# Performance work log

Hardware: AMD Instinct MI355X
Metric: run time of the kernel (lower is better)

Reference implementation:

```python
import jax, jax.numpy as jnp
import numpy as np

IMAGE_SIZE = 640
NUM_CLASSES = 80
MAX_BOXES = 100
SCORE_THR = 0.25
IOU_THR = 0.1
K_PRE = 256  # pre-NMS candidates per class (fixed-shape surrogate for tf.where filtering)
ANCHORS = np.array([[10,13],[16,30],[33,23],[30,61],[62,45],[59,119],
                    [116,90],[156,198],[373,326]], dtype=np.float32)


def setup_inputs() -> dict:
    key = jax.random.key(0)
    k5, k4, k3 = jax.random.split(key, 3)
    B = 16
    return {
        "p5": jax.random.normal(k5, (B, 20, 20, 255), dtype=jnp.float32),
        "p4": jax.random.normal(k4, (B, 40, 40, 255), dtype=jnp.float32),
        "p3": jax.random.normal(k3, (B, 80, 80, 255), dtype=jnp.float32),
    }


def _decode_layer(fm, anchors):
    # fm: [B, g, g, 3*(5+C)]; anchors: [3, 2] in input-image pixels
    B, g = fm.shape[0], fm.shape[1]
    ratio = IMAGE_SIZE / g
    fm = fm.reshape(B, g, g, 3, 5 + NUM_CLASSES)
    ctr = jax.nn.sigmoid(fm[..., :2])                      # [B,g,g,3,2]
    gx, gy = jnp.meshgrid(jnp.arange(g), jnp.arange(g))    # 'xy' indexing, same as tf
    offset = jnp.stack([gx, gy], axis=-1).astype(fm.dtype)[:, :, None, :]
    ctr = (ctr + offset) * ratio                           # pixel-space centers (x, y)
    # (anchor/ratio)*exp(t)*ratio == anchor*exp(t)
    sizes = jnp.exp(fm[..., 2:4]) * anchors                # pixel-space (w, h)
    conf = jax.nn.sigmoid(fm[..., 4:5])
    prob = jax.nn.sigmoid(fm[..., 5:])
    boxes = jnp.concatenate([ctr, sizes], axis=-1).reshape(B, -1, 4)
    scores = (conf * prob).reshape(B, -1, NUM_CLASSES)
    return boxes, scores


def _pairwise_iou(b):
    # b: [K, 4] in (x1, y1, x2, y2)
    x1, y1, x2, y2 = b[:, 0], b[:, 1], b[:, 2], b[:, 3]
    area = jnp.maximum(x2 - x1, 0.0) * jnp.maximum(y2 - y1, 0.0)
    iw = jnp.maximum(jnp.minimum(x2[:, None], x2[None, :]) - jnp.maximum(x1[:, None], x1[None, :]), 0.0)
    ih = jnp.maximum(jnp.minimum(y2[:, None], y2[None, :]) - jnp.maximum(y1[:, None], y1[None, :]), 0.0)
    inter = iw * ih
    union = area[:, None] + area[None, :] - inter
    return inter / jnp.maximum(union, 1e-9)


def _nms_class(boxes, scores):
    # boxes: [N,4], scores: [N] for one class of one image
    s = jnp.where(scores > SCORE_THR, scores, -1.0)
    top_s, top_i = jax.lax.top_k(s, K_PRE)        # score-sorted candidates
    cb = jnp.take(boxes, top_i, axis=0)           # [K_PRE, 4]
    iou = _pairwise_iou(cb)                       # [K_PRE, K_PRE]
    idx = jnp.arange(K_PRE)
    supp0 = top_s <= SCORE_THR                    # below-threshold slots start suppressed

    def body(i, supp):
        alive = ~supp[i]
        return supp | (alive & (iou[i] > IOU_THR) & (idx > i))

    supp = jax.lax.fori_loop(0, K_PRE, body, supp0)
    keep = ~supp
    # tf NMS caps output at MAX_BOXES per class (boxes are score-sorted)
    keep = keep & (jnp.cumsum(keep.astype(jnp.int32)) <= MAX_BOXES)
    kept_s = jnp.where(keep, top_s, -1.0)
    return kept_s, top_i


def _nms_image(boxes, scores):
    # boxes: [N,4], scores: [N,C]
    kept_s, top_i = jax.vmap(_nms_class, in_axes=(None, 1))(boxes, scores)  # [C,K],[C,K]
    flat_s = kept_s.reshape(-1)
    flat_i = top_i.reshape(-1)
    cls = jnp.repeat(jnp.arange(NUM_CLASSES), K_PRE)
    fs, fi = jax.lax.top_k(flat_s, MAX_BOXES)     # global top-k across all classes
    box_idx = flat_i[fi]
    valid = fs > 0.0                              # padded/suppressed slots carry -1
    out_boxes = jnp.where(valid[:, None], jnp.take(boxes, box_idx, axis=0), -1.0)
    out_scores = jnp.where(valid, fs, -1.0)
    out_labels = jnp.where(valid, cls[fi], -1).astype(jnp.int32)
    return out_boxes, out_scores, out_labels


def reference(p5, p4, p3):
    b5, s5 = _decode_layer(p5, ANCHORS[6:9])
    b4, s4 = _decode_layer(p4, ANCHORS[3:6])
    b3, s3 = _decode_layer(p3, ANCHORS[0:3])
    boxes = jnp.concatenate([b5, b4, b3], axis=1)   # [B, 25200, 4] (cx, cy, w, h)
    scores = jnp.concatenate([s5, s4, s3], axis=1)  # [B, 25200, 80]
    cx, cy, w, h = boxes[..., 0], boxes[..., 1], boxes[..., 2], boxes[..., 3]
    boxes = jnp.stack([cx - w / 2, cy - h / 2, cx + w / 2, cy + h / 2], axis=-1)
    return jax.vmap(_nms_image)(boxes, scores)      # ([B,100,4], [B,100], [B,100] int32)
```

## Files before the change

kernel.cpp:

```cpp
#include <hip/hip_runtime.h>
#include <cstdint>

#define NBOX 25200
#define NCLS 80
#define NIMG 16
#define KPRE 256
#define MAXB 100
#define SCORE_THR 0.25f
#define IOU_THR 0.1f
#define GCAP 512
#define GCAP_OLD 2048
#define NBINS_OLD 4096
#define FK 512
#define LCAP 3072
#define SCAP 24
#define CSTR 16
#define CUT 0.5f
#define BINW 0.001953125f
#define HS2 512.0f
#define RSC 262144.0f
#define BPI 394
#define FBBINS 2048

__constant__ float c_AW[9] = {10.f,16.f,33.f,30.f,62.f,59.f,116.f,156.f,373.f};
__constant__ float c_AH[9] = {13.f,30.f,23.f,61.f,45.f,119.f,90.f,198.f,326.f};

__device__ __forceinline__ float sigmoidf_(float x) { return 1.0f / (1.0f + expf(-x)); }

__device__ __forceinline__ void box_loc(int i, const float* p5, const float* p4, const float* p3,
                                        const float*& p, int& g, int& li, int& abase) {
  if (i < 1200)      { p = p5; g = 20; li = i;        abase = 6; }
  else if (i < 6000) { p = p4; g = 40; li = i - 1200; abase = 3; }
  else               { p = p3; g = 80; li = i - 6000; abase = 0; }
}

__device__ __forceinline__ float score_full(const float* p5, const float* p4, const float* p3,
                                            int b, int c, int i) {
  const float* p; int g, li, abase;
  box_loc(i, p5, p4, p3, p, g, li, abase);
  const float* f = p + (size_t)((size_t)b * g * g * 3 + li) * 85;
  return __fmul_rn(sigmoidf_(f[4]), sigmoidf_(f[5 + c]));
}

__global__ __launch_bounds__(512) void decode_push_kernel(
    const float* __restrict__ p5, const float* __restrict__ p4, const float* __restrict__ p3,
    float* __restrict__ boxes, unsigned long long* __restrict__ lists,
    uint32_t* __restrict__ cnts, uint32_t* __restrict__ ovfl)
{
  __shared__ float rec[64 * 85];
  __shared__ float conf_s[64];
  __shared__ unsigned long long slist[NCLS][SCAP];
  __shared__ uint32_t wcnt[NCLS];
  __shared__ uint32_t sbase[NCLS], sst[NCLS];
  __shared__ unsigned short pairbuf[8 * 64];

  const int bi = blockIdx.x;
  const int b = bi / BPI, r = bi - b * BPI;
  const float* p; int g, lb, s0, nb, abase;
  if (r < 19)      { p = p5; g = 20; lb = 0;    s0 = r * 64;        abase = 6; nb = 1200  - s0; }
  else if (r < 94) { p = p4; g = 40; lb = 1200; s0 = (r - 19) * 64; abase = 3; nb = 4800  - s0; }
  else             { p = p3; g = 80; lb = 6000; s0 = (r - 94) * 64; abase = 0; nb = 19200 - s0; }
  if (nb > 64) nb = 64;
  const int tid = threadIdx.x;

  if (tid < NCLS) wcnt[tid] = 0;
  {
    const float4* src4 = (const float4*)(p + ((size_t)b * g * g * 3 + s0) * 85);
    float4* rec4 = (float4*)rec;
    int n4 = nb * 85 / 4;
    for (int k = tid; k < n4; k += 512) rec4[k] = src4[k];
  }
  __syncthreads();

  if (tid < nb) {
    const float* f = rec + tid * 85;
    int li = s0 + tid;
    int cell = li / 3, a = li - cell * 3;
    float ratio = 640.0f / (float)g;
    float cx = (sigmoidf_(f[0]) + (float)(cell % g)) * ratio;
    float cy = (sigmoidf_(f[1]) + (float)(cell / g)) * ratio;
    float w = expf(f[2]) * c_AW[abase + a];
    float h = expf(f[3]) * c_AH[abase + a];
    float hw = 0.5f * w, hh = 0.5f * h;
    float4* ob = (float4*)(boxes + ((size_t)b * NBOX + lb + li) * 4);
    *ob = make_float4(cx - hw, cy - hh, cx + hw, cy + hh);
    conf_s[tid] = sigmoidf_(f[4]);
  }
  __syncthreads();

  {
    const int wave = tid >> 6, lane = tid & 63;
    const int c0 = wave * 10;
    const bool jok = lane < nb;
    float cl = jok ? rec[lane * 85 + 4] : -1.0f;
    float Lthr;
    if (!jok || cl <= 0.0f) {
      Lthr = 3.0e38f;
    } else {
      float conf = conf_s[lane];
      float u = CUT / conf;
      if (u > 0.999f) Lthr = -3.0e38f;
      else Lthr = logf(u / (1.0f - u)) - 0.01f;
    }
    const float* fl = rec + lane * 85 + 5;
    const unsigned long long lt = (lane == 0) ? 0ull : (~0ull >> (64 - lane));
    unsigned short* pb = pairbuf + (wave << 6);

    auto flushFn = [&](int mm) {
      if (lane < mm) {
        int e = pb[lane];
        int l2 = e >> 4, cc2 = e & 15;
        int c2 = c0 + cc2;
        float s = __fmul_rn(conf_s[l2], sigmoidf_(rec[l2 * 85 + 5 + c2]));
        if (s > CUT) {
          uint32_t slot = atomicAdd(&wcnt[c2], 1u);
          if (slot < SCAP)
            slist[c2][slot] = ((unsigned long long)__float_as_uint(s) << 32)
                              | (0xFFFFFFFFu - (uint32_t)(lb + s0 + l2));
        }
      }
    };

    int m = 0;
    for (int cc = 0; cc < 10; ++cc) {
      float lg = jok ? fl[c0 + cc] : -3.0e38f;
      bool cand = lg > Lthr;
      unsigned long long mk = __ballot(cand);
      int pc = __popcll(mk);
      if (m + pc > 64) { flushFn(m); m = 0; }
      if (cand) {
        int rank = __popcll(mk & lt);
        pb[m + rank] = (unsigned short)((lane << 4) | cc);
      }
      m += pc;
    }
    flushFn(m);
  }
  __syncthreads();

  if (tid < NCLS) {
    uint32_t full = wcnt[tid];
    if (full > SCAP) ovfl[b * NCLS + tid] = 1u;
    uint32_t st = full < SCAP ? full : SCAP;
    sst[tid] = st;
    sbase[tid] = atomicAdd(&cnts[(size_t)(b * NCLS + tid) * CSTR], st);
  }
  __syncthreads();

  for (int t = tid; t < NCLS * SCAP; t += 512) {
    int c = t / SCAP, k = t - c * SCAP;
    if ((uint32_t)k < sst[c]) {
      uint32_t dst = sbase[c] + (uint32_t)k;
      if (dst < LCAP)
        lists[(size_t)(b * NCLS + c) * LCAP + dst] = slist[c][k];
    }
  }
}

union ShMix2 {
  uint32_t rhist[512];
  uint32_t fhist[FBBINS];
  unsigned long long rowm[KPRE][4];
};

__global__ __launch_bounds__(512) void select_nms_list_kernel(
    const unsigned long long* __restrict__ lists, const uint32_t* __restrict__ cnts,
    const uint32_t* __restrict__ ovfl, const float* __restrict__ boxes,
    const float* __restrict__ p5, const float* __restrict__ p4, const float* __restrict__ p3,
    float* __restrict__ kept_s, int* __restrict__ top_i)
{
  const int task = blockIdx.x;
  const int b = task / NCLS, c = task - b * NCLS;
  const int tid = threadIdx.x;

  __shared__ uint32_t S[256];
  __shared__ unsigned long long keys[GCAP];
  __shared__ ShMix2 u;
  __shared__ float4 bbx[KPRE];
  __shared__ float bar_[KPRE];
  __shared__ unsigned long long suppInit[4];
  __shared__ unsigned long long sh_t[4];
  __shared__ int s_B, s_cnt, s_state, sh_stop;
  __shared__ float s_gl, s_lo, s_hi;
  __shared__ uint32_t s_above, s_g2;

  const uint32_t cntraw = cnts[(size_t)task * CSTR];
  bool fb = (ovfl[task] != 0u) || !(cntraw >= (uint32_t)KPRE && cntraw <= (uint32_t)LCAP);
  float thr = CUT;
  int n_all = (int)(cntraw < (uint32_t)LCAP ? cntraw : (uint32_t)LCAP);
  const unsigned long long* gl = lists + (size_t)task * LCAP;

  if (!fb && n_all > 500) {
    if (tid < 256) S[tid] = 0;
    __syncthreads();
    for (int z = tid; z < n_all; z += 512) {
      float s = __uint_as_float((uint32_t)(gl[z] >> 32));
      int bin = (int)(__fmul_rn(__fsub_rn(s, CUT), HS2));
      bin = bin < 0 ? 0 : (bin > 255 ? 255 : bin);
      atomicAdd(&S[bin], 1u);
    }
    __syncthreads();
    for (int off = 1; off < 256; off <<= 1) {
      uint32_t add = 0;
      if (tid < 256 && tid + off < 256) add = S[tid + off];
      __syncthreads();
      if (tid < 256) S[tid] += add;
      __syncthreads();
    }
    if (tid == 0) s_B = 0;
    __syncthreads();
    if (tid < 256) {
      uint32_t Sz = S[tid];
      uint32_t Sz1 = (tid < 255) ? S[tid + 1] : 0u;
      if (Sz >= KPRE && (tid == 255 || Sz1 < KPRE)) s_B = tid;
    }
    __syncthreads();
    const int B = s_B;
    const uint32_t gcount = S[B];
    const uint32_t aboveB = (B < 255) ? S[B + 1] : 0u;
    thr = CUT + (float)B * BINW;
    if (gcount > 500u) {
      for (int z = tid; z < 512; z += 512) u.rhist[z] = 0u;
      __syncthreads();
      float rLo = thr;
      for (int z = tid; z < n_all; z += 512) {
        float s = __uint_as_float((uint32_t)(gl[z] >> 32));
        int bin = (int)(__fmul_rn(__fsub_rn(s, CUT), HS2));
        bin = bin < 0 ? 0 : (bin > 255 ? 255 : bin);
        if (bin == B) {
          int sub = (int)((s - rLo) * RSC);
          sub = sub < 0 ? 0 : (sub > 511 ? 511 : sub);
          atomicAdd(&u.rhist[sub], 1u);
        }
      }
      __syncthreads();
// ... 73 lines not shown
  __syncthreads();
  if (!fb) {
    for (int z = tid; z < n_all; z += 512) {
      unsigned long long kk = gl[z];
      float s = __uint_as_float((uint32_t)(kk >> 32));
      if (s > thr_n) {
        int slot = atomicAdd(&s_cnt, 1);
        if (slot < GCAP) keys[slot] = kk;
      }
    }
  } else {
    for (int i = tid; i < NBOX; i += 512) {
      float s = score_full(p5, p4, p3, b, c, i);
      if (s > thr_n && s > SCORE_THR) {
        int slot = atomicAdd(&s_cnt, 1);
        if (slot < GCAP)
          keys[slot] = ((unsigned long long)__float_as_uint(s) << 32) | (0xFFFFFFFFu - (uint32_t)i);
      }
    }
  }
  __syncthreads();
  int n = s_cnt < GCAP ? s_cnt : GCAP;
  if (tid >= n) keys[tid] = 0ull;
  __syncthreads();
  {
    unsigned long long v = keys[tid];
    for (int k = 2; k <= GCAP; k <<= 1) {
      for (int j = k >> 1; j > 0; j >>= 1) {
        unsigned long long pv;
        if (j >= 64) {
          keys[tid] = v;
          __syncthreads();
          pv = keys[tid ^ j];
          __syncthreads();
        } else {
          pv = __shfl_xor(v, j, 64);
        }
        bool takeMax = (((tid & k) == 0) == ((tid & j) == 0));
        v = takeMax ? (v > pv ? v : pv) : (v < pv ? v : pv);
      }
    }
    keys[tid] = v;
  }
  __syncthreads();

  const int col = tid & 255;
  float sc; int idx;
  {
    unsigned long long kk = keys[col];
    if ((uint32_t)(kk >> 32) != 0u) { sc = __uint_as_float((uint32_t)(kk >> 32)); idx = (int)(0xFFFFFFFFu - (uint32_t)kk); }
    else { sc = -1.0f; idx = 0; }
  }
  if (tid < KPRE) {
    const float* bp = boxes + ((size_t)b * NBOX + idx) * 4;
    float bx1 = bp[0], by1 = bp[1], bx2 = bp[2], by2 = bp[3];
    bbx[tid] = make_float4(bx1, by1, bx2, by2);
    bar_[tid] = __fmul_rn(fmaxf(__fsub_rn(bx2, bx1), 0.0f), fmaxf(__fsub_rn(by2, by1), 0.0f));
  }
  {
    unsigned long long alive = __ballot(sc > SCORE_THR);
    if (tid < KPRE && (tid & 63) == 0) suppInit[tid >> 6] = ~alive;
  }
  if (tid == 0) sh_stop = 0;
  __syncthreads();
  float4 MB = bbx[col];
  float x1 = MB.x, y1 = MB.y, x2 = MB.z, y2 = MB.w;
  float area = bar_[col];
  if (tid < 4) sh_t[tid] = suppInit[tid];
  __syncthreads();

  int P = 4;
  const int rg = tid >> 8;
  #pragma unroll
  for (int q = 0; q < 4; ++q) {
    for (int ii = 0; ii < 64; ii += 2) {
      int i = q * 64 + ii + rg;
      if (!((sh_t[q] >> (ii + rg)) & 1ull)) {
        float4 B = bbx[i];
        float ar = bar_[i];
        float iw = fmaxf(__fsub_rn(fminf(x2, B.z), fmaxf(x1, B.x)), 0.0f);
        float ih = fmaxf(__fsub_rn(fminf(y2, B.w), fmaxf(y1, B.y)), 0.0f);
        float inter = __fmul_rn(iw, ih);
        float ab = __fadd_rn(ar, area);
        float diff = __fsub_rn(__fmul_rn(inter, 1.1f), __fmul_rn(0.1f, ab));
        bool sup;
        if (fabsf(diff) > 1e-5f * ab) {
          sup = diff > 0.0f;
        } else {
          float uni = __fsub_rn(ab, inter);
          sup = (inter / fmaxf(uni, 1e-9f)) > IOU_THR;
        }
        sup = sup && (col > i);
        unsigned long long m = __ballot(sup);
        if ((tid & 63) == 0) u.rowm[i][(tid >> 6) & 3] = m;
      }
    }
    __syncthreads();
    if (tid == 0) {
      unsigned long long t0 = sh_t[0], t1 = sh_t[1], t2 = sh_t[2], t3 = sh_t[3];
      for (int ii = 0; ii < 64; ++ii) {
        int i = q * 64 + ii;
        unsigned long long cur = (q == 0) ? t0 : (q == 1) ? t1 : (q == 2) ? t2 : t3;
        if (!((cur >> ii) & 1ull)) {
          if (q <= 0) t0 |= u.rowm[i][0];
          if (q <= 1) t1 |= u.rowm[i][1];
          if (q <= 2) t2 |= u.rowm[i][2];
          t3 |= u.rowm[i][3];
        }
      }
      sh_t[0] = t0; sh_t[1] = t1; sh_t[2] = t2; sh_t[3] = t3;
      int kept = __popcll(~t0);
      if (q >= 1) kept += __popcll(~t1);
      if (q >= 2) kept += __popcll(~t2);
      if (q >= 3) kept += __popcll(~t3);
      if (kept >= MAXB) sh_stop = 1;
    }
    __syncthreads();
    if (sh_stop) { P = q + 1; break; }
  }

  if (tid < KPRE) {
    unsigned long long tw = sh_t[tid >> 6];
    bool kept = (tid < 64 * P) && !((tw >> (tid & 63)) & 1ull);
    int rank = 0;
    #pragma unroll
    for (int w2 = 0; w2 < 4; ++w2)
      if (w2 < (tid >> 6)) rank += __popcll(~sh_t[w2]);
    int l = tid & 63;
    rank += (l == 0) ? 0 : __popcll(~tw & ((~0ull) >> (64 - l)));
    bool fin = kept && (rank < MAXB);
    kept_s[(size_t)task * KPRE + tid] = fin ? sc : -1.0f;
    top_i[(size_t)task * KPRE + tid] = idx;
  }
}

__global__ __launch_bounds__(256) void decode_kernel(
    const float* __restrict__ p5, const float* __restrict__ p4, const float* __restrict__ p3,
    float* __restrict__ boxes, float* __restrict__ conf)
{
  int t = blockIdx.x * 256 + threadIdx.x;
  if (t >= NIMG * NBOX) return;
  int b = t / NBOX, i = t - b * NBOX;
  const float* p; int g, li, abase;
  box_loc(i, p5, p4, p3, p, g, li, abase);
  int cell = li / 3, a = li - cell * 3;
  float ratio = 640.0f / (float)g;
  const float* f = p + ((size_t)((size_t)b * g * g + cell) * 255 + a * 85);
  float cx = (sigmoidf_(f[0]) + (float)(cell % g)) * ratio;
  float cy = (sigmoidf_(f[1]) + (float)(cell / g)) * ratio;
  float w = expf(f[2]) * c_AW[abase + a];
  float h = expf(f[3]) * c_AH[abase + a];
  float hw = 0.5f * w, hh = 0.5f * h;
  float* ob = boxes + (size_t)t * 4;
  ob[0] = cx - hw; ob[1] = cy - hh; ob[2] = cx + hw; ob[3] = cy + hh;
  conf[t] = sigmoidf_(f[4]);
}

__device__ __forceinline__ float score_at(
    const float* __restrict__ p5, const float* __restrict__ p4, const float* __restrict__ p3,
    const float* __restrict__ conf, int b, int c, int i)
{
  const float* p; int g, li, abase;
  box_loc(i, p5, p4, p3, p, g, li, abase);
  float logit = p[(size_t)((size_t)b * g * g * 3 + li) * 85 + 5 + c];
  return __fmul_rn(conf[b * NBOX + i], 1.0f / (1.0f + expf(-logit)));
}

__global__ __launch_bounds__(256) void select_nms_kernel(
    const float* __restrict__ p5, const float* __restrict__ p4, const float* __restrict__ p3,
    const float* __restrict__ conf, const float* __restrict__ boxes,
    float* __restrict__ kept_s, int* __restrict__ top_i)
{
  const int task = blockIdx.x;
  const int b = task / NCLS, c = task - b * NCLS;
  const int tid = threadIdx.x;
  __shared__ uint32_t hist[NBINS_OLD];
  __shared__ uint32_t chunkS[256];
  __shared__ unsigned long long keys[GCAP_OLD];
  __shared__ float s_lo, s_hi, s_glo;
  __shared__ uint32_t s_above;
  __shared__ int s_state, s_cnt;

  float lo = SCORE_THR, hi = 1.0f;
  uint32_t above = 0;
  float gatherLo = SCORE_THR;
  bool done = false;
  for (int iter = 0; iter < 6 && !done; ++iter) {
    for (int z = tid; z < NBINS_OLD; z += 256) hist[z] = 0;
    __syncthreads();
    float scale = (float)NBINS_OLD / (hi - lo);
    for (int i = tid; i < NBOX; i += 256) {
      float s = score_at(p5, p4, p3, conf, b, c, i);
      if (s > lo && s <= hi) {
        int bin = (int)((s - lo) * scale);
        bin = bin < 0 ? 0 : (bin > NBINS_OLD - 1 ? NBINS_OLD - 1 : bin);
        atomicAdd(&hist[bin], 1u);
      }
    }
    __syncthreads();
    { uint32_t cs = 0; int base = tid * 16;
      #pragma unroll
      for (int z = 0; z < 16; ++z) cs += hist[base + z];
      chunkS[tid] = cs; }
    __syncthreads();
    if (tid == 0) {
      uint32_t acc = 0; int ch;
      for (ch = 255; ch >= 0; --ch) {
        if (above + acc + chunkS[ch] >= KPRE) break;
// ... 42 lines not shown
          unsigned long long a0 = keys[i2], b0_ = keys[ixj];
          bool sw = ((i2 & k) == 0) ? (a0 < b0_) : (a0 > b0_);
          if (sw) { keys[i2] = b0_; keys[ixj] = a0; }
        }
      }
      __syncthreads();
    }
  }
  __shared__ float bx1[KPRE], by1[KPRE], bx2[KPRE], by2[KPRE], bar_[KPRE], tsc[KPRE];
  __shared__ int tix[KPRE];
  __shared__ unsigned char suppA[KPRE], keepA[KPRE];
  { int r = tid;
    unsigned long long kk = keys[r];
    float sc; int idx;
    if ((uint32_t)(kk >> 32) != 0u) { sc = __uint_as_float((uint32_t)(kk >> 32)); idx = (int)(0xFFFFFFFFu - (uint32_t)kk); }
    else { sc = -1.0f; idx = 0; }
    tsc[r] = sc; tix[r] = idx;
    const float* bp = boxes + ((size_t)b * NBOX + idx) * 4;
    float x1 = bp[0], y1 = bp[1], x2 = bp[2], y2 = bp[3];
    bx1[r] = x1; by1[r] = y1; bx2[r] = x2; by2[r] = y2;
    bar_[r] = __fmul_rn(fmaxf(__fsub_rn(x2, x1), 0.0f), fmaxf(__fsub_rn(y2, y1), 0.0f));
    suppA[r] = (sc <= SCORE_THR) ? 1 : 0; }
  __syncthreads();
  for (int i = 0; i < KPRE; ++i) {
    if (suppA[i] == 0) {
      int r = tid;
      if (r > i) {
        float iw = fmaxf(__fsub_rn(fminf(bx2[r], bx2[i]), fmaxf(bx1[r], bx1[i])), 0.0f);
        float ih = fmaxf(__fsub_rn(fminf(by2[r], by2[i]), fmaxf(by1[r], by1[i])), 0.0f);
        float inter = __fmul_rn(iw, ih);
        float uni = __fsub_rn(__fadd_rn(bar_[r], bar_[i]), inter);
        float iou = inter / fmaxf(uni, 1e-9f);
        if (iou > IOU_THR) suppA[r] = 1;
      }
    }
    __syncthreads();
  }
  if (tid == 0) {
    int cnt = 0;
    for (int r = 0; r < KPRE; ++r) {
      int kp = (suppA[r] == 0) ? 1 : 0;
      if (kp && cnt < MAXB) cnt++; else kp = 0;
      keepA[r] = (unsigned char)kp;
    }
  }
  __syncthreads();
  { int r = tid;
    kept_s[(size_t)task * KPRE + r] = keepA[r] ? tsc[r] : -1.0f;
    top_i[(size_t)task * KPRE + r] = tix[r]; }
}

__global__ __launch_bounds__(256) void final_topk_kernel(
    const float* __restrict__ kept_s, const int* __restrict__ top_i,
    const float* __restrict__ boxes, float* __restrict__ out)
{
  int b = blockIdx.x, tid = threadIdx.x;
  __shared__ uint32_t hist[NBINS_OLD];
  __shared__ uint32_t chunkS[256];
  __shared__ unsigned long long keys[FK];
  __shared__ float s_lo, s_hi, s_glo;
  __shared__ uint32_t s_above;
  __shared__ int s_state, s_cnt;
  const float* ks = kept_s + (size_t)b * NCLS * KPRE;
  const int NK = NCLS * KPRE;

  float lo = SCORE_THR, hi = 1.0f;
  uint32_t above = 0;
  float gatherLo = SCORE_THR;
  bool done = false;

  for (int iter = 0; iter < 4 && !done; ++iter) {
    for (int z = tid; z < NBINS_OLD; z += 256) hist[z] = 0;
    __syncthreads();
    float scale = (float)NBINS_OLD / (hi - lo);
    for (int z = tid; z < NK; z += 256) {
      float s = ks[z];
      if (s > lo && s <= hi) {
        int bin = (int)((s - lo) * scale);
        bin = bin < 0 ? 0 : (bin > NBINS_OLD - 1 ? NBINS_OLD - 1 : bin);
        atomicAdd(&hist[bin], 1u);
      }
    }
    __syncthreads();
    {
      uint32_t cs = 0; int base = tid * 16;
      #pragma unroll
      for (int z = 0; z < 16; ++z) cs += hist[base + z];
      chunkS[tid] = cs;
    }
    __syncthreads();
    if (tid == 0) {
      uint32_t acc = 0; int ch;
      for (ch = 255; ch >= 0; --ch) {
        if (above + acc + chunkS[ch] >= MAXB) break;
        acc += chunkS[ch];
      }
      if (ch < 0) { s_state = 1; s_glo = SCORE_THR; }
      else {
        int B = -1;
        for (int z = ch * 16 + 15; z >= ch * 16; --z) {
          acc += hist[z];
          if (above + acc >= MAXB) { B = z; break; }
        }
        uint32_t popB = hist[B];
        uint32_t aboveNew = above + acc - popB;
        float wdt = (hi - lo) / (float)NBINS_OLD;
        float binLo = lo + (float)B * wdt;
        if (aboveNew + popB <= (uint32_t)(FK - 64) || iter == 3) { s_state = 1; s_glo = binLo; }
        else { s_state = 0; s_lo = binLo; s_hi = binLo + wdt; s_above = aboveNew; }
      }
    }
    __syncthreads();
    if (s_state == 1) { gatherLo = s_glo; done = true; }
    else { lo = s_lo; hi = s_hi; above = s_above; }
    __syncthreads();
  }
  gatherLo = __uint_as_float(__float_as_uint(gatherLo) - 8u);

  if (tid == 0) s_cnt = 0;
  __syncthreads();
  for (int z = tid; z < NK; z += 256) {
    float s = ks[z];
    if (s > gatherLo && s > 0.0f) {
      int slot = atomicAdd(&s_cnt, 1);
      if (slot < FK)
        keys[slot] = ((unsigned long long)__float_as_uint(s) << 32) | (uint32_t)(0xFFFFFFFFu - (uint32_t)z);
    }
  }
  __syncthreads();
  int n = s_cnt < FK ? s_cnt : FK;
  for (int z = tid; z < FK; z += 256) if (z >= n) keys[z] = 0ull;
  __syncthreads();
  for (int k = 2; k <= FK; k <<= 1) {
    for (int j = k >> 1; j > 0; j >>= 1) {
      for (int i2 = tid; i2 < FK; i2 += 256) {
        int ixj = i2 ^ j;
        if (ixj > i2) {
          unsigned long long a0 = keys[i2], b0_ = keys[ixj];
          bool sw = ((i2 & k) == 0) ? (a0 < b0_) : (a0 > b0_);
          if (sw) { keys[i2] = b0_; keys[ixj] = a0; }
        }
      }
      __syncthreads();
    }
  }
  float* ob = out + (size_t)b * MAXB * 4;
  float* os = out + (size_t)NIMG * MAXB * 4 + (size_t)b * MAXB;
  float* ol = out + (size_t)NIMG * MAXB * 4 + (size_t)NIMG * MAXB + (size_t)b * MAXB;
  for (int t = tid; t < MAXB; t += 256) {
    unsigned long long kk = keys[t];
    if ((uint32_t)(kk >> 32) != 0u) {
      float s = __uint_as_float((uint32_t)(kk >> 32));
      int fr = (int)(0xFFFFFFFFu - (uint32_t)kk);
      int cc = fr >> 8, rr = fr & 255;
      int idx = top_i[((size_t)b * NCLS + cc) * KPRE + rr];
      const float* bp = boxes + ((size_t)b * NBOX + idx) * 4;
      ob[t * 4 + 0] = bp[0]; ob[t * 4 + 1] = bp[1]; ob[t * 4 + 2] = bp[2]; ob[t * 4 + 3] = bp[3];
      os[t] = s; ol[t] = (float)cc;
    } else {
      ob[t * 4 + 0] = -1.0f; ob[t * 4 + 1] = -1.0f; ob[t * 4 + 2] = -1.0f; ob[t * 4 + 3] = -1.0f;
      os[t] = -1.0f; ol[t] = -1.0f;
    }
  }
}

extern "C" void kernel_launch(void* const* d_in, const int* in_sizes, int n_in,
                              void* d_out, int out_size, void* d_ws, size_t ws_size,
                              hipStream_t stream)
{
  const float* p5 = (const float*)d_in[0];
  const float* p4 = (const float*)d_in[1];
  const float* p3 = (const float*)d_in[2];
  float* out = (float*)d_out;

  float*    boxes = (float*)d_ws;
  float*    kept  = boxes + (size_t)NIMG * NBOX * 4;
  int*      topi  = (int*)(kept + (size_t)NIMG * NCLS * KPRE);
  uint32_t* cnts  = (uint32_t*)(topi + (size_t)NIMG * NCLS * KPRE);
  uint32_t* ovfl  = cnts + (size_t)NIMG * NCLS * CSTR;
  unsigned long long* lists = (unsigned long long*)(ovfl + NIMG * NCLS);

  size_t need_main = ((size_t)NIMG * NBOX * 4 + (size_t)NIMG * NCLS * KPRE * 2
                      + (size_t)NIMG * NCLS * CSTR + (size_t)NIMG * NCLS) * 4
                     + (size_t)NIMG * NCLS * LCAP * 8;

  if (ws_size >= need_main) {
    hipMemsetAsync(cnts, 0, (size_t)NIMG * NCLS * (CSTR + 1) * sizeof(uint32_t), stream);
    decode_push_kernel<<<NIMG * BPI, 512, 0, stream>>>(p5, p4, p3, boxes, lists, cnts, ovfl);
    select_nms_list_kernel<<<NIMG * NCLS, 512, 0, stream>>>(lists, cnts, ovfl, boxes, p5, p4, p3, kept, topi);
  } else {
    float* conf = (float*)(cnts);
    decode_kernel<<<(NIMG * NBOX + 255) / 256, 256, 0, stream>>>(p5, p4, p3, boxes, conf);
    select_nms_kernel<<<NIMG * NCLS, 256, 0, stream>>>(p5, p4, p3, conf, boxes, kept, topi);
  }
  final_topk_kernel<<<NIMG, 256, 0, stream>>>(kept, topi, boxes, out);
}
```

Measured before the change: 209.9 us.

## Decode boxes on demand and fuse final top-k into last NMS block

Stops materialising the full decoded box array in the decode kernel. Boxes are recomputed from the raw feature maps only for the candidates NMS and the output need. The final per-image top-k is folded into the select/NMS kernel through a last-block-done atomic counter, which removes one kernel launch. The serial single-thread suppression scan becomes a wave-wide scan using shuffles. In exchange it adds redundant sigmoid/exp work, a threadfence and atomic per block, and a serial tail done by the last block of each image.

```diff
diff --git a/kernel.cpp b/kernel.cpp
--- a/kernel.cpp
+++ b/kernel.cpp
@@ -42,13 +42,27 @@
   return __fmul_rn(sigmoidf_(f[4]), sigmoidf_(f[5 + c]));
 }
 
+__device__ __forceinline__ float4 decode_box(const float* p5, const float* p4, const float* p3,
+                                             int b, int i) {
+  const float* p; int g, li, abase;
+  box_loc(i, p5, p4, p3, p, g, li, abase);
+  const float* f = p + (size_t)((size_t)b * g * g * 3 + li) * 85;
+  int cell = li / 3, a = li - cell * 3;
+  float ratio = 640.0f / (float)g;
+  float cx = (sigmoidf_(f[0]) + (float)(cell % g)) * ratio;
+  float cy = (sigmoidf_(f[1]) + (float)(cell / g)) * ratio;
+  float w = expf(f[2]) * c_AW[abase + a];
+  float h = expf(f[3]) * c_AH[abase + a];
+  float hw = 0.5f * w, hh = 0.5f * h;
+  return make_float4(cx - hw, cy - hh, cx + hw, cy + hh);
+}
+
 __global__ __launch_bounds__(512) void decode_push_kernel(
     const float* __restrict__ p5, const float* __restrict__ p4, const float* __restrict__ p3,
-    float* __restrict__ boxes, unsigned long long* __restrict__ lists,
-    uint32_t* __restrict__ cnts, uint32_t* __restrict__ ovfl)
+    unsigned long long* __restrict__ lists, uint32_t* __restrict__ cnts,
+    uint32_t* __restrict__ ovfl)
 {
   __shared__ float rec[64 * 85];
-  __shared__ float conf_s[64];
   __shared__ unsigned long long slist[NCLS][SCAP];
   __shared__ uint32_t wcnt[NCLS];
   __shared__ uint32_t sbase[NCLS], sst[NCLS];
@@ -56,10 +70,10 @@
 
   const int bi = blockIdx.x;
   const int b = bi / BPI, r = bi - b * BPI;
-  const float* p; int g, lb, s0, nb, abase;
-  if (r < 19)      { p = p5; g = 20; lb = 0;    s0 = r * 64;        abase = 6; nb = 1200  - s0; }
-  else if (r < 94) { p = p4; g = 40; lb = 1200; s0 = (r - 19) * 64; abase = 3; nb = 4800  - s0; }
-  else             { p = p3; g = 80; lb = 6000; s0 = (r - 94) * 64; abase = 0; nb = 19200 - s0; }
+  const float* p; int g, lb, s0, nb;
+  if (r < 19)      { p = p5; g = 20; lb = 0;    s0 = r * 64;        nb = 1200  - s0; }
+  else if (r < 94) { p = p4; g = 40; lb = 1200; s0 = (r - 19) * 64; nb = 4800  - s0; }
+  else             { p = p3; g = 80; lb = 6000; s0 = (r - 94) * 64; nb = 19200 - s0; }
   if (nb > 64) nb = 64;
   const int tid = threadIdx.x;
 
@@ -69,22 +83,6 @@
     float4* rec4 = (float4*)rec;
     int n4 = nb * 85 / 4;
     for (int k = tid; k < n4; k += 512) rec4[k] = src4[k];
-  }
-  __syncthreads();
-
-  if (tid < nb) {
-    const float* f = rec + tid * 85;
-    int li = s0 + tid;
-    int cell = li / 3, a = li - cell * 3;
-    float ratio = 640.0f / (float)g;
-    float cx = (sigmoidf_(f[0]) + (float)(cell % g)) * ratio;
-    float cy = (sigmoidf_(f[1]) + (float)(cell / g)) * ratio;
-    float w = expf(f[2]) * c_AW[abase + a];
-    float h = expf(f[3]) * c_AH[abase + a];
-    float hw = 0.5f * w, hh = 0.5f * h;
-    float4* ob = (float4*)(boxes + ((size_t)b * NBOX + lb + li) * 4);
-    *ob = make_float4(cx - hw, cy - hh, cx + hw, cy + hh);
-    conf_s[tid] = sigmoidf_(f[4]);
   }
   __syncthreads();
 
@@ -97,10 +95,10 @@
     if (!jok || cl <= 0.0f) {
       Lthr = 3.0e38f;
     } else {
-      float conf = conf_s[lane];
-      float u = CUT / conf;
-      if (u > 0.999f) Lthr = -3.0e38f;
-      else Lthr = logf(u / (1.0f - u)) - 0.01f;
+      float conf = 1.0f / (1.0f + expf(-cl));
+      float u2 = CUT / conf;
+      if (u2 > 0.999f) Lthr = -3.0e38f;
+      else Lthr = logf(u2 / (1.0f - u2)) - 0.01f;
     }
     const float* fl = rec + lane * 85 + 5;
     const unsigned long long lt = (lane == 0) ? 0ull : (~0ull >> (64 - lane));
@@ -111,7 +109,7 @@
         int e = pb[lane];
         int l2 = e >> 4, cc2 = e & 15;
         int c2 = c0 + cc2;
-        float s = __fmul_rn(conf_s[l2], sigmoidf_(rec[l2 * 85 + 5 + c2]));
+        float s = __fmul_rn(sigmoidf_(rec[l2 * 85 + 4]), sigmoidf_(rec[l2 * 85 + 5 + c2]));
         if (s > CUT) {
           uint32_t slot = atomicAdd(&wcnt[c2], 1u);
           if (slot < SCAP)
@@ -165,9 +163,10 @@
 
 __global__ __launch_bounds__(512) void select_nms_list_kernel(
     const unsigned long long* __restrict__ lists, const uint32_t* __restrict__ cnts,
-    const uint32_t* __restrict__ ovfl, const float* __restrict__ boxes,
+    const uint32_t* __restrict__ ovfl,
     const float* __restrict__ p5, const float* __restrict__ p4, const float* __restrict__ p3,
-    float* __restrict__ kept_s, int* __restrict__ top_i)
+    float* __restrict__ kept_s, int* __restrict__ top_i,
+    uint32_t* __restrict__ imgcnt, float* __restrict__ out)
 {
   const int task = blockIdx.x;
   const int b = task / NCLS, c = task - b * NCLS;
@@ -180,7 +179,7 @@
   __shared__ float bar_[KPRE];
   __shared__ unsigned long long suppInit[4];
   __shared__ unsigned long long sh_t[4];
-  __shared__ int s_B, s_cnt, s_state, sh_stop;
+  __shared__ int s_B, s_cnt, s_state, sh_stop, sh_last;
   __shared__ float s_gl, s_lo, s_hi;
   __shared__ uint32_t s_above, s_g2;
 
@@ -360,10 +359,9 @@
     else { sc = -1.0f; idx = 0; }
   }
   if (tid < KPRE) {
-    const float* bp = boxes + ((size_t)b * NBOX + idx) * 4;
-    float bx1 = bp[0], by1 = bp[1], bx2 = bp[2], by2 = bp[3];
-    bbx[tid] = make_float4(bx1, by1, bx2, by2);
-    bar_[tid] = __fmul_rn(fmaxf(__fsub_rn(bx2, bx1), 0.0f), fmaxf(__fsub_rn(by2, by1), 0.0f));
+    float4 bx = decode_box(p5, p4, p3, b, idx);
+    bbx[tid] = bx;
+    bar_[tid] = __fmul_rn(fmaxf(__fsub_rn(bx.z, bx.x), 0.0f), fmaxf(__fsub_rn(bx.w, bx.y), 0.0f));
   }
   {
     unsigned long long alive = __ballot(sc > SCORE_THR);
@@ -404,24 +402,28 @@
       }
     }
     __syncthreads();
-    if (tid == 0) {
+    if (tid < 64) {
+      unsigned long long r0 = u.rowm[q * 64 + tid][0];
+      unsigned long long r1 = u.rowm[q * 64 + tid][1];
+      unsigned long long r2 = u.rowm[q * 64 + tid][2];
+      unsigned long long r3 = u.rowm[q * 64 + tid][3];
       unsigned long long t0 = sh_t[0], t1 = sh_t[1], t2 = sh_t[2], t3 = sh_t[3];
+      unsigned long long tq = (q == 0) ? t0 : (q == 1) ? t1 : (q == 2) ? t2 : t3;
       for (int ii = 0; ii < 64; ++ii) {
-        int i = q * 64 + ii;
-        unsigned long long cur = (q == 0) ? t0 : (q == 1) ? t1 : (q == 2) ? t2 : t3;
-        if (!((cur >> ii) & 1ull)) {
-          if (q <= 0) t0 |= u.rowm[i][0];
-          if (q <= 1) t1 |= u.rowm[i][1];
-          if (q <= 2) t2 |= u.rowm[i][2];
-          t3 |= u.rowm[i][3];
-        }
-      }
-      sh_t[0] = t0; sh_t[1] = t1; sh_t[2] = t2; sh_t[3] = t3;
-      int kept = __popcll(~t0);
-      if (q >= 1) kept += __popcll(~t1);
-      if (q >= 2) kept += __popcll(~t2);
-      if (q >= 3) kept += __popcll(~t3);
-      if (kept >= MAXB) sh_stop = 1;
+        if (!((tq >> ii) & 1ull)) {
+          t0 |= __shfl(r0, ii); t1 |= __shfl(r1, ii);
+          t2 |= __shfl(r2, ii); t3 |= __shfl(r3, ii);
+          tq = (q == 0) ? t0 : (q == 1) ? t1 : (q == 2) ? t2 : t3;
+        }
+      }
+      if (tid == 0) {
+        sh_t[0] = t0; sh_t[1] = t1; sh_t[2] = t2; sh_t[3] = t3;
+        int kept = __popcll(~t0);
+        if (q >= 1) kept += __popcll(~t1);
+        if (q >= 2) kept += __popcll(~t2);
+        if (q >= 3) kept += __popcll(~t3);
+        if (kept >= MAXB) sh_stop = 1;
+      }
     }
     __syncthreads();
     if (sh_stop) { P = q + 1; break; }
@@ -440,6 +442,125 @@
     kept_s[(size_t)task * KPRE + tid] = fin ? sc : -1.0f;
     top_i[(size_t)task * KPRE + tid] = idx;
   }
+
+  __threadfence();
+  __syncthreads();
+  if (tid == 0) {
+    uint32_t done = atomicAdd(&imgcnt[b], 1u);
+    sh_last = (done == (uint32_t)(NCLS - 1)) ? 1 : 0;
+  }
+  __syncthreads();
+  if (!sh_last) return;
+  __threadfence();
+
+  const float* ks = kept_s + (size_t)b * NCLS * KPRE;
+  const int NK = NCLS * KPRE;
+  {
+    float lo = SCORE_THR, hi = 1.0f;
+    uint32_t above = 0;
+    float gLo = SCORE_THR;
+    bool done2 = false;
+    for (int iter = 0; iter < 4 && !done2; ++iter) {
+      for (int z = tid; z < FBBINS; z += 512) u.fhist[z] = 0u;
+      __syncthreads();
+      float scale = (float)FBBINS / (hi - lo);
+      for (int z = tid; z < NK; z += 512) {
+        float s = ks[z];
+        if (s > lo && s <= hi) {
+          int bin = (int)((s - lo) * scale);
+          bin = bin < 0 ? 0 : (bin > FBBINS - 1 ? FBBINS - 1 : bin);
+          atomicAdd(&u.fhist[bin], 1u);
+        }
+      }
+      __syncthreads();
+      if (tid < 256) {
+        uint32_t cs = 0; int base = tid * 8;
+        #pragma unroll
+        for (int z = 0; z < 8; ++z) cs += u.fhist[base + z];
+        S[tid] = cs;
+      }
+      __syncthreads();
+      if (tid == 0) {
+        uint32_t acc = 0; int ch;
+        for (ch = 255; ch >= 0; --ch) {
+          if (above + acc + S[ch] >= MAXB) break;
+          acc += S[ch];
+        }
+        if (ch < 0) { s_state = 1; s_gl = SCORE_THR; }
+        else {
+          int B = -1;
+          for (int z = ch * 8 + 7; z >= ch * 8; --z) {
+            acc += u.fhist[z];
+            if (above + acc >= MAXB) { B = z; break; }
+          }
+          uint32_t popB = u.fhist[B];
+          uint32_t aboveNew = above + acc - popB;
+          float wdt = (hi - lo) / (float)FBBINS;
+          float binLo = lo + (float)B * wdt;
+          if (aboveNew + popB <= (uint32_t)(FK - 64) || iter == 3) { s_state = 1; s_gl = binLo; }
+          else { s_state = 0; s_lo = binLo; s_hi = binLo + wdt; s_above = aboveNew; }
+        }
+      }
+      __syncthreads();
+      if (s_state == 1) { gLo = s_gl; done2 = true; }
+      else { lo = s_lo; hi = s_hi; above = s_above; }
+      __syncthreads();
+    }
+    float gLo_n = __uint_as_float(__float_as_uint(gLo) - 8u);
+
+    if (tid == 0) s_cnt = 0;
+    __syncthreads();
+    for (int z = tid; z < NK; z += 512) {
+      float s = ks[z];
+      if (s > gLo_n && s > 0.0f) {
+        int slot = atomicAdd(&s_cnt, 1);
+        if (slot < FK)
+          keys[slot] = ((unsigned long long)__float_as_uint(s) << 32) | (uint32_t)(0xFFFFFFFFu - (uint32_t)z);
+      }
+    }
+    __syncthreads();
+    int n2 = s_cnt < FK ? s_cnt : FK;
+    if (tid >= n2) keys[tid] = 0ull;
+    __syncthreads();
+    {
+      unsigned long long v = keys[tid];
+      for (int k = 2; k <= FK; k <<= 1) {
+        for (int j = k >> 1; j > 0; j >>= 1) {
+          unsigned long long pv;
+          if (j >= 64) {
+            keys[tid] = v;
+            __syncthreads();
+            pv = keys[tid ^ j];
+            __syncthreads();
+          } else {
+            pv = __shfl_xor(v, j, 64);
+          }
+          bool takeMax = (((tid & k) == 0) == ((tid & j) == 0));
+          v = takeMax ? (v > pv ? v : pv) : (v < pv ? v : pv);
+        }
+      }
+      keys[tid] = v;
+    }
+    __syncthreads();
+    float* ob = out + (size_t)b * MAXB * 4;
+    float* os = out + (size_t)NIMG * MAXB * 4 + (size_t)b * MAXB;
+    float* ol = out + (size_t)NIMG * MAXB * 4 + (size_t)NIMG * MAXB + (size_t)b * MAXB;
+    for (int t = tid; t < MAXB; t += 512) {
+      unsigned long long kk = keys[t];
+      if ((uint32_t)(kk >> 32) != 0u) {
+        float s = __uint_as_float((uint32_t)(kk >> 32));
+        int fr = (int)(0xFFFFFFFFu - (uint32_t)kk);
+        int cc = fr >> 8, rr = fr & 255;
+        int bidx = top_i[((size_t)b * NCLS + cc) * KPRE + rr];
+        float4 bx = decode_box(p5, p4, p3, b, bidx);
+        ob[t * 4 + 0] = bx.x; ob[t * 4 + 1] = bx.y; ob[t * 4 + 2] = bx.z; ob[t * 4 + 3] = bx.w;
+        os[t] = s; ol[t] = (float)cc;
+      } else {
+        ob[t * 4 + 0] = -1.0f; ob[t * 4 + 1] = -1.0f; ob[t * 4 + 2] = -1.0f; ob[t * 4 + 3] = -1.0f;
+        os[t] = -1.0f; ol[t] = -1.0f;
+      }
+    }
+  }
 }
 
 __global__ __launch_bounds__(256) void decode_kernel(
@@ -449,19 +570,12 @@
   int t = blockIdx.x * 256 + threadIdx.x;
   if (t >= NIMG * NBOX) return;
   int b = t / NBOX, i = t - b * NBOX;
+  float4 bx = decode_box(p5, p4, p3, b, i);
+  float* ob = boxes + (size_t)t * 4;
+  ob[0] = bx.x; ob[1] = bx.y; ob[2] = bx.z; ob[3] = bx.w;
   const float* p; int g, li, abase;
   box_loc(i, p5, p4, p3, p, g, li, abase);
-  int cell = li / 3, a = li - cell * 3;
-  float ratio = 640.0f / (float)g;
-  const float* f = p + ((size_t)((size_t)b * g * g + cell) * 255 + a * 85);
-  float cx = (sigmoidf_(f[0]) + (float)(cell % g)) * ratio;
-  float cy = (sigmoidf_(f[1]) + (float)(cell / g)) * ratio;
-  float w = expf(f[2]) * c_AW[abase + a];
-  float h = expf(f[3]) * c_AH[abase + a];
-  float hw = 0.5f * w, hh = 0.5f * h;
-  float* ob = boxes + (size_t)t * 4;
-  ob[0] = cx - hw; ob[1] = cy - hh; ob[2] = cx + hw; ob[3] = cy + hh;
-  conf[t] = sigmoidf_(f[4]);
+  conf[t] = sigmoidf_(p[(size_t)((size_t)b * g * g * 3 + li) * 85 + 4]);
 }
 
 __device__ __forceinline__ float score_at(
@@ -610,7 +724,8 @@
 
 __global__ __launch_bounds__(256) void final_topk_kernel(
     const float* __restrict__ kept_s, const int* __restrict__ top_i,
-    const float* __restrict__ boxes, float* __restrict__ out)
+    const float* __restrict__ p5, const float* __restrict__ p4, const float* __restrict__ p3,
+    float* __restrict__ out)
 {
   int b = blockIdx.x, tid = threadIdx.x;
   __shared__ uint32_t hist[NBINS_OLD];
@@ -712,8 +827,8 @@
       int fr = (int)(0xFFFFFFFFu - (uint32_t)kk);
       int cc = fr >> 8, rr = fr & 255;
       int idx = top_i[((size_t)b * NCLS + cc) * KPRE + rr];
-      const float* bp = boxes + ((size_t)b * NBOX + idx) * 4;
-      ob[t * 4 + 0] = bp[0]; ob[t * 4 + 1] = bp[1]; ob[t * 4 + 2] = bp[2]; ob[t * 4 + 3] = bp[3];
+      float4 bx = decode_box(p5, p4, p3, b, idx);
+      ob[t * 4 + 0] = bx.x; ob[t * 4 + 1] = bx.y; ob[t * 4 + 2] = bx.z; ob[t * 4 + 3] = bx.w;
       os[t] = s; ol[t] = (float)cc;
     } else {
       ob[t * 4 + 0] = -1.0f; ob[t * 4 + 1] = -1.0f; ob[t * 4 + 2] = -1.0f; ob[t * 4 + 3] = -1.0f;
@@ -731,25 +846,29 @@
   const float* p3 = (const float*)d_in[2];
   float* out = (float*)d_out;
 
-  float*    boxes = (float*)d_ws;
-  float*    kept  = boxes + (size_t)NIMG * NBOX * 4;
-  int*      topi  = (int*)(kept + (size_t)NIMG * NCLS * KPRE);
-  uint32_t* cnts  = (uint32_t*)(topi + (size_t)NIMG * NCLS * KPRE);
-  uint32_t* ovfl  = cnts + (size_t)NIMG * NCLS * CSTR;
-  unsigned long long* lists = (unsigned long long*)(ovfl + NIMG * NCLS);
+  float*    boxes  = (float*)d_ws;
+  float*    kept   = boxes + (size_t)NIMG * NBOX * 4;
+  int*      topi   = (int*)(kept + (size_t)NIMG * NCLS * KPRE);
+  uint32_t* cnts   = (uint32_t*)(topi + (size_t)NIMG * NCLS * KPRE);
+  uint32_t* ovfl   = cnts + (size_t)NIMG * NCLS * CSTR;
+  uint32_t* imgcnt = ovfl + NIMG * NCLS;
+  unsigned long long* lists = (unsigned long long*)(imgcnt + NIMG);
 
   size_t need_main = ((size_t)NIMG * NBOX * 4 + (size_t)NIMG * NCLS * KPRE * 2
-                      + (size_t)NIMG * NCLS * CSTR + (size_t)NIMG * NCLS) * 4
+                      + (size_t)NIMG * NCLS * CSTR + (size_t)NIMG * NCLS + NIMG) * 4
                      + (size_t)NIMG * NCLS * LCAP * 8;
 
   if (ws_size >= need_main) {
-    hipMemsetAsync(cnts, 0, (size_t)NIMG * NCLS * (CSTR + 1) * sizeof(uint32_t), stream);
-    decode_push_kernel<<<NIMG * BPI, 512, 0, stream>>>(p5, p4, p3, boxes, lists, cnts, ovfl);
-    select_nms_list_kernel<<<NIMG * NCLS, 512, 0, stream>>>(lists, cnts, ovfl, boxes, p5, p4, p3, kept, topi);
+    hipMemsetAsync(cnts, 0,
+                   ((size_t)NIMG * NCLS * CSTR + (size_t)NIMG * NCLS + NIMG) * sizeof(uint32_t),
+                   stream);
+    decode_push_kernel<<<NIMG * BPI, 512, 0, stream>>>(p5, p4, p3, lists, cnts, ovfl);
+    select_nms_list_kernel<<<NIMG * NCLS, 512, 0, stream>>>(lists, cnts, ovfl, p5, p4, p3,
+                                                            kept, topi, imgcnt, out);
   } else {
-    float* conf = (float*)(cnts);
+    float* conf = (float*)lists;
     decode_kernel<<<(NIMG * NBOX + 255) / 256, 256, 0, stream>>>(p5, p4, p3, boxes, conf);
     select_nms_kernel<<<NIMG * NCLS, 256, 0, stream>>>(p5, p4, p3, conf, boxes, kept, topi);
-  }
-  final_topk_kernel<<<NIMG, 256, 0, stream>>>(kept, topi, boxes, out);
-}
+    final_topk_kernel<<<NIMG, 256, 0, stream>>>(kept, topi, p5, p4, p3, out);
+  }
+}
```

New measurement: 335.4 us. 59.8% more time.

## Decode boxes on demand instead of materializing box buffer; parallelize NMS sweep

Applied to the files above, without the earlier changes.

The decode-push kernel no longer writes the full decoded box array or a per-box confidence buffer. The NMS and final top-k kernels instead recompute each candidate box from the raw feature maps when they need it. The serial single-thread suppression sweep over row masks becomes a wave-wide loop that pulls row masks through shuffles. This removes a large global write and a later scattered read, at the cost of extra transcendental math and scattered raw-feature reads per candidate. The fallback path now puts the conf buffer in the lists region.

```diff
diff --git a/kernel.cpp b/kernel.cpp
--- a/kernel.cpp
+++ b/kernel.cpp
@@ -42,13 +42,27 @@
   return __fmul_rn(sigmoidf_(f[4]), sigmoidf_(f[5 + c]));
 }
 
+__device__ __forceinline__ float4 decode_box(const float* p5, const float* p4, const float* p3,
+                                             int b, int i) {
+  const float* p; int g, li, abase;
+  box_loc(i, p5, p4, p3, p, g, li, abase);
+  const float* f = p + (size_t)((size_t)b * g * g * 3 + li) * 85;
+  int cell = li / 3, a = li - cell * 3;
+  float ratio = 640.0f / (float)g;
+  float cx = (sigmoidf_(f[0]) + (float)(cell % g)) * ratio;
+  float cy = (sigmoidf_(f[1]) + (float)(cell / g)) * ratio;
+  float w = expf(f[2]) * c_AW[abase + a];
+  float h = expf(f[3]) * c_AH[abase + a];
+  float hw = 0.5f * w, hh = 0.5f * h;
+  return make_float4(cx - hw, cy - hh, cx + hw, cy + hh);
+}
+
 __global__ __launch_bounds__(512) void decode_push_kernel(
     const float* __restrict__ p5, const float* __restrict__ p4, const float* __restrict__ p3,
-    float* __restrict__ boxes, unsigned long long* __restrict__ lists,
-    uint32_t* __restrict__ cnts, uint32_t* __restrict__ ovfl)
+    unsigned long long* __restrict__ lists, uint32_t* __restrict__ cnts,
+    uint32_t* __restrict__ ovfl)
 {
   __shared__ float rec[64 * 85];
-  __shared__ float conf_s[64];
   __shared__ unsigned long long slist[NCLS][SCAP];
   __shared__ uint32_t wcnt[NCLS];
   __shared__ uint32_t sbase[NCLS], sst[NCLS];
@@ -56,10 +70,10 @@
 
   const int bi = blockIdx.x;
   const int b = bi / BPI, r = bi - b * BPI;
-  const float* p; int g, lb, s0, nb, abase;
-  if (r < 19)      { p = p5; g = 20; lb = 0;    s0 = r * 64;        abase = 6; nb = 1200  - s0; }
-  else if (r < 94) { p = p4; g = 40; lb = 1200; s0 = (r - 19) * 64; abase = 3; nb = 4800  - s0; }
-  else             { p = p3; g = 80; lb = 6000; s0 = (r - 94) * 64; abase = 0; nb = 19200 - s0; }
+  const float* p; int g, lb, s0, nb;
+  if (r < 19)      { p = p5; g = 20; lb = 0;    s0 = r * 64;        nb = 1200  - s0; }
+  else if (r < 94) { p = p4; g = 40; lb = 1200; s0 = (r - 19) * 64; nb = 4800  - s0; }
+  else             { p = p3; g = 80; lb = 6000; s0 = (r - 94) * 64; nb = 19200 - s0; }
   if (nb > 64) nb = 64;
   const int tid = threadIdx.x;
 
@@ -69,22 +83,6 @@
     float4* rec4 = (float4*)rec;
     int n4 = nb * 85 / 4;
     for (int k = tid; k < n4; k += 512) rec4[k] = src4[k];
-  }
-  __syncthreads();
-
-  if (tid < nb) {
-    const float* f = rec + tid * 85;
-    int li = s0 + tid;
-    int cell = li / 3, a = li - cell * 3;
-    float ratio = 640.0f / (float)g;
-    float cx = (sigmoidf_(f[0]) + (float)(cell % g)) * ratio;
-    float cy = (sigmoidf_(f[1]) + (float)(cell / g)) * ratio;
-    float w = expf(f[2]) * c_AW[abase + a];
-    float h = expf(f[3]) * c_AH[abase + a];
-    float hw = 0.5f * w, hh = 0.5f * h;
-    float4* ob = (float4*)(boxes + ((size_t)b * NBOX + lb + li) * 4);
-    *ob = make_float4(cx - hw, cy - hh, cx + hw, cy + hh);
-    conf_s[tid] = sigmoidf_(f[4]);
   }
   __syncthreads();
 
@@ -97,10 +95,10 @@
     if (!jok || cl <= 0.0f) {
       Lthr = 3.0e38f;
     } else {
-      float conf = conf_s[lane];
-      float u = CUT / conf;
-      if (u > 0.999f) Lthr = -3.0e38f;
-      else Lthr = logf(u / (1.0f - u)) - 0.01f;
+      float conf = 1.0f / (1.0f + expf(-cl));
+      float u2 = CUT / conf;
+      if (u2 > 0.999f) Lthr = -3.0e38f;
+      else Lthr = logf(u2 / (1.0f - u2)) - 0.01f;
     }
     const float* fl = rec + lane * 85 + 5;
     const unsigned long long lt = (lane == 0) ? 0ull : (~0ull >> (64 - lane));
@@ -111,7 +109,7 @@
         int e = pb[lane];
         int l2 = e >> 4, cc2 = e & 15;
         int c2 = c0 + cc2;
-        float s = __fmul_rn(conf_s[l2], sigmoidf_(rec[l2 * 85 + 5 + c2]));
+        float s = __fmul_rn(sigmoidf_(rec[l2 * 85 + 4]), sigmoidf_(rec[l2 * 85 + 5 + c2]));
         if (s > CUT) {
           uint32_t slot = atomicAdd(&wcnt[c2], 1u);
           if (slot < SCAP)
@@ -165,7 +163,7 @@
 
 __global__ __launch_bounds__(512) void select_nms_list_kernel(
     const unsigned long long* __restrict__ lists, const uint32_t* __restrict__ cnts,
-    const uint32_t* __restrict__ ovfl, const float* __restrict__ boxes,
+    const uint32_t* __restrict__ ovfl,
     const float* __restrict__ p5, const float* __restrict__ p4, const float* __restrict__ p3,
     float* __restrict__ kept_s, int* __restrict__ top_i)
 {
@@ -360,10 +358,9 @@
     else { sc = -1.0f; idx = 0; }
   }
   if (tid < KPRE) {
-    const float* bp = boxes + ((size_t)b * NBOX + idx) * 4;
-    float bx1 = bp[0], by1 = bp[1], bx2 = bp[2], by2 = bp[3];
-    bbx[tid] = make_float4(bx1, by1, bx2, by2);
-    bar_[tid] = __fmul_rn(fmaxf(__fsub_rn(bx2, bx1), 0.0f), fmaxf(__fsub_rn(by2, by1), 0.0f));
+    float4 bx = decode_box(p5, p4, p3, b, idx);
+    bbx[tid] = bx;
+    bar_[tid] = __fmul_rn(fmaxf(__fsub_rn(bx.z, bx.x), 0.0f), fmaxf(__fsub_rn(bx.w, bx.y), 0.0f));
   }
   {
     unsigned long long alive = __ballot(sc > SCORE_THR);
@@ -404,24 +401,28 @@
       }
     }
     __syncthreads();
-    if (tid == 0) {
+    if (tid < 64) {
+      unsigned long long r0 = u.rowm[q * 64 + tid][0];
+      unsigned long long r1 = u.rowm[q * 64 + tid][1];
+      unsigned long long r2 = u.rowm[q * 64 + tid][2];
+      unsigned long long r3 = u.rowm[q * 64 + tid][3];
       unsigned long long t0 = sh_t[0], t1 = sh_t[1], t2 = sh_t[2], t3 = sh_t[3];
+      unsigned long long tq = (q == 0) ? t0 : (q == 1) ? t1 : (q == 2) ? t2 : t3;
       for (int ii = 0; ii < 64; ++ii) {
-        int i = q * 64 + ii;
-        unsigned long long cur = (q == 0) ? t0 : (q == 1) ? t1 : (q == 2) ? t2 : t3;
-        if (!((cur >> ii) & 1ull)) {
-          if (q <= 0) t0 |= u.rowm[i][0];
-          if (q <= 1) t1 |= u.rowm[i][1];
-          if (q <= 2) t2 |= u.rowm[i][2];
-          t3 |= u.rowm[i][3];
-        }
-      }
-      sh_t[0] = t0; sh_t[1] = t1; sh_t[2] = t2; sh_t[3] = t3;
-      int kept = __popcll(~t0);
-      if (q >= 1) kept += __popcll(~t1);
-      if (q >= 2) kept += __popcll(~t2);
-      if (q >= 3) kept += __popcll(~t3);
-      if (kept >= MAXB) sh_stop = 1;
+        if (!((tq >> ii) & 1ull)) {
+          t0 |= __shfl(r0, ii); t1 |= __shfl(r1, ii);
+          t2 |= __shfl(r2, ii); t3 |= __shfl(r3, ii);
+          tq = (q == 0) ? t0 : (q == 1) ? t1 : (q == 2) ? t2 : t3;
+        }
+      }
+      if (tid == 0) {
+        sh_t[0] = t0; sh_t[1] = t1; sh_t[2] = t2; sh_t[3] = t3;
+        int kept = __popcll(~t0);
+        if (q >= 1) kept += __popcll(~t1);
+        if (q >= 2) kept += __popcll(~t2);
+        if (q >= 3) kept += __popcll(~t3);
+        if (kept >= MAXB) sh_stop = 1;
+      }
     }
     __syncthreads();
     if (sh_stop) { P = q + 1; break; }
@@ -449,19 +450,12 @@
   int t = blockIdx.x * 256 + threadIdx.x;
   if (t >= NIMG * NBOX) return;
   int b = t / NBOX, i = t - b * NBOX;
+  float4 bx = decode_box(p5, p4, p3, b, i);
+  float* ob = boxes + (size_t)t * 4;
+  ob[0] = bx.x; ob[1] = bx.y; ob[2] = bx.z; ob[3] = bx.w;
   const float* p; int g, li, abase;
   box_loc(i, p5, p4, p3, p, g, li, abase);
-  int cell = li / 3, a = li - cell * 3;
-  float ratio = 640.0f / (float)g;
-  const float* f = p + ((size_t)((size_t)b * g * g + cell) * 255 + a * 85);
-  float cx = (sigmoidf_(f[0]) + (float)(cell % g)) * ratio;
-  float cy = (sigmoidf_(f[1]) + (float)(cell / g)) * ratio;
-  float w = expf(f[2]) * c_AW[abase + a];
-  float h = expf(f[3]) * c_AH[abase + a];
-  float hw = 0.5f * w, hh = 0.5f * h;
-  float* ob = boxes + (size_t)t * 4;
-  ob[0] = cx - hw; ob[1] = cy - hh; ob[2] = cx + hw; ob[3] = cy + hh;
-  conf[t] = sigmoidf_(f[4]);
+  conf[t] = sigmoidf_(p[(size_t)((size_t)b * g * g * 3 + li) * 85 + 4]);
 }
 
 __device__ __forceinline__ float score_at(
@@ -610,7 +604,8 @@
 
 __global__ __launch_bounds__(256) void final_topk_kernel(
     const float* __restrict__ kept_s, const int* __restrict__ top_i,
-    const float* __restrict__ boxes, float* __restrict__ out)
+    const float* __restrict__ p5, const float* __restrict__ p4, const float* __restrict__ p3,
+    float* __restrict__ out)
 {
   int b = blockIdx.x, tid = threadIdx.x;
   __shared__ uint32_t hist[NBINS_OLD];
@@ -712,8 +707,8 @@
       int fr = (int)(0xFFFFFFFFu - (uint32_t)kk);
       int cc = fr >> 8, rr = fr & 255;
       int idx = top_i[((size_t)b * NCLS + cc) * KPRE + rr];
-      const float* bp = boxes + ((size_t)b * NBOX + idx) * 4;
-      ob[t * 4 + 0] = bp[0]; ob[t * 4 + 1] = bp[1]; ob[t * 4 + 2] = bp[2]; ob[t * 4 + 3] = bp[3];
+      float4 bx = decode_box(p5, p4, p3, b, idx);
+      ob[t * 4 + 0] = bx.x; ob[t * 4 + 1] = bx.y; ob[t * 4 + 2] = bx.z; ob[t * 4 + 3] = bx.w;
       os[t] = s; ol[t] = (float)cc;
     } else {
       ob[t * 4 + 0] = -1.0f; ob[t * 4 + 1] = -1.0f; ob[t * 4 + 2] = -1.0f; ob[t * 4 + 3] = -1.0f;
@@ -731,11 +726,11 @@
   const float* p3 = (const float*)d_in[2];
   float* out = (float*)d_out;
 
-  float*    boxes = (float*)d_ws;
-  float*    kept  = boxes + (size_t)NIMG * NBOX * 4;
-  int*      topi  = (int*)(kept + (size_t)NIMG * NCLS * KPRE);
-  uint32_t* cnts  = (uint32_t*)(topi + (size_t)NIMG * NCLS * KPRE);
-  uint32_t* ovfl  = cnts + (size_t)NIMG * NCLS * CSTR;
+  float*    boxes  = (float*)d_ws;
+  float*    kept   = boxes + (size_t)NIMG * NBOX * 4;
+  int*      topi   = (int*)(kept + (size_t)NIMG * NCLS * KPRE);
+  uint32_t* cnts   = (uint32_t*)(topi + (size_t)NIMG * NCLS * KPRE);
+  uint32_t* ovfl   = cnts + (size_t)NIMG * NCLS * CSTR;
   unsigned long long* lists = (unsigned long long*)(ovfl + NIMG * NCLS);
 
   size_t need_main = ((size_t)NIMG * NBOX * 4 + (size_t)NIMG * NCLS * KPRE * 2
@@ -743,13 +738,16 @@
                      + (size_t)NIMG * NCLS * LCAP * 8;
 
   if (ws_size >= need_main) {
-    hipMemsetAsync(cnts, 0, (size_t)NIMG * NCLS * (CSTR + 1) * sizeof(uint32_t), stream);
-    decode_push_kernel<<<NIMG * BPI, 512, 0, stream>>>(p5, p4, p3, boxes, lists, cnts, ovfl);
-    select_nms_list_kernel<<<NIMG * NCLS, 512, 0, stream>>>(lists, cnts, ovfl, boxes, p5, p4, p3, kept, topi);
+    hipMemsetAsync(cnts, 0,
+                   ((size_t)NIMG * NCLS * CSTR + (size_t)NIMG * NCLS) * sizeof(uint32_t),
+                   stream);
+    decode_push_kernel<<<NIMG * BPI, 512, 0, stream>>>(p5, p4, p3, lists, cnts, ovfl);
+    select_nms_list_kernel<<<NIMG * NCLS, 512, 0, stream>>>(lists, cnts, ovfl, p5, p4, p3,
+                                                            kept, topi);
   } else {
-    float* conf = (float*)(cnts);
+    float* conf = (float*)lists;
     decode_kernel<<<(NIMG * NBOX + 255) / 256, 256, 0, stream>>>(p5, p4, p3, boxes, conf);
     select_nms_kernel<<<NIMG * NCLS, 256, 0, stream>>>(p5, p4, p3, conf, boxes, kept, topi);
   }
-  final_topk_kernel<<<NIMG, 256, 0, stream>>>(kept, topi, boxes, out);
-}
+  final_topk_kernel<<<NIMG, 256, 0, stream>>>(kept, topi, p5, p4, p3, out);
+}
```

Measured after the change: 216.7 us. 1.03x slower.
